# Kernel tuning notes

Hardware: AMD Instinct MI355X
Metric: run time of the kernel (lower is better)

Reference implementation:

```python
import jax, jax.numpy as jnp
import numpy as np

B, T, C, H = 2, 2048, 1024, 16

def setup_inputs() -> dict:
    key = jax.random.key(0)
    ks = jax.random.split(key, 6)
    s = 1.0 / np.sqrt(C)
    return {
        "x": jax.random.normal(ks[0], (B, T, C), jnp.float32),
        "Wq": jax.random.normal(ks[1], (C, C), jnp.float32) * s,
        "Wk": jax.random.normal(ks[2], (C, C), jnp.float32) * s,
        "Wv": jax.random.normal(ks[3], (C, C), jnp.float32) * s,
        "Wp": jax.random.normal(ks[4], (C, C), jnp.float32) * s,
        "bp": jnp.zeros((C,), jnp.float32),
    }

def reference(x, Wq, Wk, Wv, Wp, bp):
    b, t, c = x.shape
    hd = c // H  # head dim
    # Linear layers: torch nn.Linear computes x @ W.T
    def split_heads(y):
        return y.reshape(b, t, H, hd).transpose(0, 2, 1, 3)  # [B,H,T,hd]
    q = split_heads(x @ Wq.T)
    k = split_heads(x @ Wk.T)
    v = split_heads(x @ Wv.T)
    scale = hd ** -0.5
    wei = jnp.einsum('bhqd,bhkd->bhqk', q, k) * scale  # [B,H,T,T]
    causal = jnp.tril(jnp.ones((t, t), bool))
    wei = jnp.where(causal, wei, -jnp.inf)
    wei = jax.nn.softmax(wei, axis=-1)
    out = jnp.einsum('bhqk,bhkd->bhqd', wei, v)  # [B,H,T,hd]
    out = out.transpose(0, 2, 1, 3).reshape(b, t, c)
    return out @ Wp.T + bp
```

## Files before the change

### kernel.cpp

```cpp
#include <hip/hip_runtime.h>
#include <hip/hip_bf16.h>
#include <stdint.h>

#define B_ 2
#define T_ 2048
#define C_ 1024
#define H_ 16
#define HD_ 64
#define NTOK (B_*T_)

typedef __bf16 bf16;
typedef bf16 bf16x4 __attribute__((ext_vector_type(4)));
typedef bf16 bf16x8 __attribute__((ext_vector_type(8)));
typedef float f32x4 __attribute__((ext_vector_type(4)));

static __device__ __forceinline__ f32x4 mfma16(bf16x8 a, bf16x8 b, f32x4 c) {
  return __builtin_amdgcn_mfma_f32_16x16x32_bf16(a, b, c, 0, 0, 0);
}

static __device__ __forceinline__ void gload_lds16(const void* g, void* l) {
  __builtin_amdgcn_global_load_lds(
      (__attribute__((address_space(1))) void*)g,
      (__attribute__((address_space(3))) void*)l, 16, 0, 0);
}

static __device__ __forceinline__ uint32_t cvt_pk_bf16(float lo, float hi) {
  uint32_t r;
  asm("v_cvt_pk_bf16_f32 %0, %1, %2" : "=v"(r) : "v"(lo), "v"(hi));
  return r;
}

__global__ void cvt_f32_bf16(const float* __restrict__ src, bf16* __restrict__ dst, int n4) {
  int i = blockIdx.x * blockDim.x + threadIdx.x;
  if (i >= n4) return;
  float4 v = reinterpret_cast<const float4*>(src)[i];
  bf16x4 o;
  o.x = (bf16)v.x; o.y = (bf16)v.y; o.z = (bf16)v.z; o.w = (bf16)v.w;
  reinterpret_cast<bf16x4*>(dst)[i] = o;
}

__global__ void cvt4_f32_bf16(const float* __restrict__ s0, const float* __restrict__ s1,
                              const float* __restrict__ s2, const float* __restrict__ s3,
                              bf16* __restrict__ d0, bf16* __restrict__ d1,
                              bf16* __restrict__ d2, bf16* __restrict__ d3, int n4) {
  int i = blockIdx.x * blockDim.x + threadIdx.x;
  if (i >= n4) return;
  const float* src = (blockIdx.y == 0) ? s0 : (blockIdx.y == 1) ? s1 : (blockIdx.y == 2) ? s2 : s3;
  bf16* dst = (blockIdx.y == 0) ? d0 : (blockIdx.y == 1) ? d1 : (blockIdx.y == 2) ? d2 : d3;
  float4 v = reinterpret_cast<const float4*>(src)[i];
  bf16x4 o;
  o.x = (bf16)v.x; o.y = (bf16)v.y; o.z = (bf16)v.z; o.w = (bf16)v.w;
  reinterpret_cast<bf16x4*>(dst)[i] = o;
}

__global__ __launch_bounds__(256) void qkv_gemm(
    const bf16* __restrict__ X,
    const bf16* __restrict__ Wq, const bf16* __restrict__ Wk, const bf16* __restrict__ Wv,
    bf16* __restrict__ Q, bf16* __restrict__ K, bf16* __restrict__ VT) {
  __shared__ bf16 As[128 * 32];
  __shared__ bf16 Bs[128 * 32];
  const int z = blockIdx.z;
  const bf16* W = (z == 0) ? Wq : (z == 1) ? Wk : Wv;
  const int n0 = blockIdx.x * 128;
  const int o0 = blockIdx.y * 128;
  const int tid = threadIdx.x;
  const int lane = tid & 63;
  const int w = tid >> 6;
  const int wr = w >> 1, wc = w & 1;
  const int l15 = lane & 15, lhi = lane >> 4;

  f32x4 acc[4][4] = {};

  const int ca = tid;
  const int cb = tid + 256;
  const int rowa = ca >> 2, cola = (ca & 3) * 8;
  const int rowb = cb >> 2, colb = (cb & 3) * 8;

  for (int k0 = 0; k0 < C_; k0 += 32) {
    __syncthreads();
    gload_lds16(X + (size_t)(n0 + rowa) * C_ + k0 + cola, (char*)As + ca * 16);
    gload_lds16(X + (size_t)(n0 + rowb) * C_ + k0 + colb, (char*)As + cb * 16);
    gload_lds16(W + (size_t)(o0 + rowa) * C_ + k0 + cola, (char*)Bs + ca * 16);
    gload_lds16(W + (size_t)(o0 + rowb) * C_ + k0 + colb, (char*)Bs + cb * 16);
    __syncthreads();
    bf16x8 a[4], b[4];
#pragma unroll
    for (int m = 0; m < 4; m++)
      a[m] = *reinterpret_cast<const bf16x8*>(&As[(wr * 64 + m * 16 + l15) * 32 + lhi * 8]);
#pragma unroll
    for (int n = 0; n < 4; n++)
      b[n] = *reinterpret_cast<const bf16x8*>(&Bs[(wc * 64 + n * 16 + l15) * 32 + lhi * 8]);
#pragma unroll
    for (int m = 0; m < 4; m++)
#pragma unroll
      for (int n = 0; n < 4; n++)
        acc[m][n] = mfma16(a[m], b[n], acc[m][n]);
  }

  const float QSCALE = 0.125f * 1.44269504f;
#pragma unroll
  for (int m = 0; m < 4; m++) {
#pragma unroll
    for (int n = 0; n < 4; n++) {
#pragma unroll
      for (int r = 0; r < 4; r++) {
        int tok = n0 + wr * 64 + m * 16 + lhi * 4 + r;
        int o = o0 + wc * 64 + n * 16 + l15;
        int bb = tok >> 11, t = tok & (T_ - 1);
        int h = o >> 6, d = o & 63;
        float v = acc[m][n][r];
        if (z == 0) {
          Q[((size_t)(bb * H_ + h) * T_ + t) * HD_ + d] = (bf16)(v * QSCALE);
        } else if (z == 1) {
          K[((size_t)(bb * H_ + h) * T_ + t) * HD_ + d] = (bf16)v;
        } else {
          VT[((size_t)(bb * H_ + h) * HD_ + d) * T_ + t] = (bf16)v;
        }
      }
    }
  }
}

__global__ __launch_bounds__(256, 3) void attn_kernel(
    const bf16* __restrict__ Q, const bf16* __restrict__ K,
    const bf16* __restrict__ VT, bf16* __restrict__ att) {
  __shared__ bf16 Kt[2][64 * 64];
  __shared__ bf16 Vt[2][64 * 64];
  __shared__ bf16 P[4][32][72];
  const int tid = threadIdx.x;
  const int lane = tid & 63;
  const int w = tid >> 6;
  const int l15 = lane & 15, lhi = lane >> 4;
  const int bh = blockIdx.x;
  const int b = bh >> 4, h = bh & 15;
  const int qt = (int)gridDim.y - 1 - (int)blockIdx.y;
  const int qw0 = qt * 128 + w * 32;
  const bf16* Qb = Q + (size_t)bh * T_ * HD_;
  const bf16* Kb = K + (size_t)bh * T_ * HD_;
  const bf16* Vb = VT + (size_t)bh * HD_ * T_;

  bf16x8 q[2][2];
#pragma unroll
  for (int m = 0; m < 2; m++)
#pragma unroll
    for (int kk = 0; kk < 2; kk++)
      q[m][kk] = *reinterpret_cast<const bf16x8*>(
          &Qb[(size_t)(qw0 + m * 16 + l15) * HD_ + kk * 32 + lhi * 8]);

  f32x4 o_acc[2][4] = {};
  float lsum[2] = {0.f, 0.f};

  const int nt = 2 * qt + 2;

  const int c0 = tid, c1 = tid + 256;
  const int r0 = c0 >> 3, x0 = (c0 & 7) ^ (r0 & 7);
  const int r1 = c1 >> 3, x1 = (c1 & 7) ^ (r1 & 7);

#define STAGE(tt, bb)                                                                \
  do {                                                                               \
    int kv = (tt) * 64;                                                              \
    gload_lds16(Kb + (size_t)(kv + r0) * HD_ + x0 * 8, (char*)&Kt[bb][0] + c0 * 16); \
    gload_lds16(Kb + (size_t)(kv + r1) * HD_ + x1 * 8, (char*)&Kt[bb][0] + c1 * 16); \
    gload_lds16(Vb + (size_t)r0 * T_ + kv + x0 * 8, (char*)&Vt[bb][0] + c0 * 16);    \
    gload_lds16(Vb + (size_t)r1 * T_ + kv + x1 * 8, (char*)&Vt[bb][0] + c1 * 16);    \
  } while (0)

  STAGE(0, 0);
  __syncthreads();
  int cur = 0;

  for (int it = 0; it < nt; ++it) {
    const int kv0 = it * 64;
    if (it + 1 < nt) STAGE(it + 1, cur ^ 1);

    if (kv0 <= qw0 + 31) {
      f32x4 s[2][4] = {};
#pragma unroll
      for (int n = 0; n < 4; n++) {
        const int krow = n * 16 + l15;
#pragma unroll
        for (int kk = 0; kk < 2; kk++) {
          const int kx = (kk * 4 + lhi) ^ (l15 & 7);
          bf16x8 kf = *reinterpret_cast<const bf16x8*>(
              (const char*)&Kt[cur][0] + krow * 128 + kx * 16);
          s[0][n] = mfma16(kf, q[0][kk], s[0][n]);
          s[1][n] = mfma16(kf, q[1][kk], s[1][n]);
        }
      }

      if (kv0 + 63 > qw0) {
#pragma unroll
        for (int m = 0; m < 2; m++) {
          const int qrow = qw0 + m * 16 + l15;
#pragma unroll
          for (int n = 0; n < 4; n++) {
            const int key = kv0 + n * 16 + lhi * 4;
#pragma unroll
            for (int r = 0; r < 4; r++) {
              if (key + r > qrow) s[m][n][r] = -1e30f;
            }
          }
        }
      }
#pragma unroll
      for (int m = 0; m < 2; m++) {
        char* pw = (char*)&P[w][m * 16 + l15][0];
#pragma unroll
        for (int n = 0; n < 4; n++) {
          float p0 = __builtin_amdgcn_exp2f(s[m][n][0]);
          float p1 = __builtin_amdgcn_exp2f(s[m][n][1]);
          float p2 = __builtin_amdgcn_exp2f(s[m][n][2]);
          float p3 = __builtin_amdgcn_exp2f(s[m][n][3]);
          lsum[m] += (p0 + p1) + (p2 + p3);
          uint32_t lo = cvt_pk_bf16(p0, p1);
          uint32_t hi = cvt_pk_bf16(p2, p3);
          *reinterpret_cast<uint2*>(pw + (4 * n + lhi) * 8) = make_uint2(lo, hi);
        }
      }
      bf16x8 pa[2][2];
#pragma unroll
      for (int m = 0; m < 2; m++)
#pragma unroll
        for (int kk = 0; kk < 2; kk++)
          pa[m][kk] = *reinterpret_cast<const bf16x8*>(
              (const char*)&P[w][m * 16 + l15][0] + kk * 64 + lhi * 16);
#pragma unroll
      for (int n = 0; n < 4; n++) {
        const int vrow = n * 16 + l15;
#pragma unroll
        for (int kk = 0; kk < 2; kk++) {
          const int vx = (kk * 4 + lhi) ^ (l15 & 7);
          bf16x8 vf = *reinterpret_cast<const bf16x8*>(
              (const char*)&Vt[cur][0] + vrow * 128 + vx * 16);
          o_acc[0][n] = mfma16(pa[0][kk], vf, o_acc[0][n]);
          o_acc[1][n] = mfma16(pa[1][kk], vf, o_acc[1][n]);
        }
      }
    }
    __syncthreads();
    cur ^= 1;
  }
#undef STAGE

  float lred[2];
#pragma unroll
  for (int m = 0; m < 2; m++) {
    float v = lsum[m];
    v += __shfl_xor(v, 16);
    v += __shfl_xor(v, 32);
    lred[m] = v;
  }
#pragma unroll
  for (int m = 0; m < 2; m++) {
#pragma unroll
    for (int r = 0; r < 4; r++) {
      float rs = __shfl(lred[m], (lane & 48) + lhi * 4 + r);
      float li = 1.f / rs;
      int t = qw0 + m * 16 + lhi * 4 + r;
#pragma unroll
      for (int n = 0; n < 4; n++) {
        int d = n * 16 + l15;
        att[((size_t)(b * T_ + t) * H_ + h) * HD_ + d] = (bf16)(o_acc[m][n][r] * li);
      }
    }
  }
}

__global__ __launch_bounds__(256) void proj_gemm(
    const bf16* __restrict__ A, const bf16* __restrict__ Wp,
    const float* __restrict__ bp, float* __restrict__ out) {
  __shared__ bf16 As[128 * 32];
  __shared__ bf16 Bs[128 * 32];
  const int n0 = blockIdx.x * 128;
  const int o0 = blockIdx.y * 128;
  const int tid = threadIdx.x;
  const int lane = tid & 63;
  const int w = tid >> 6;
  const int wr = w >> 1, wc = w & 1;
  const int l15 = lane & 15, lhi = lane >> 4;

  f32x4 acc[4][4] = {};

  const int ca = tid;
  const int cb = tid + 256;
  const int rowa = ca >> 2, cola = (ca & 3) * 8;
  const int rowb = cb >> 2, colb = (cb & 3) * 8;

  for (int k0 = 0; k0 < C_; k0 += 32) {
    __syncthreads();
    gload_lds16(A + (size_t)(n0 + rowa) * C_ + k0 + cola, (char*)As + ca * 16);
    gload_lds16(A + (size_t)(n0 + rowb) * C_ + k0 + colb, (char*)As + cb * 16);
    gload_lds16(Wp + (size_t)(o0 + rowa) * C_ + k0 + cola, (char*)Bs + ca * 16);
    gload_lds16(Wp + (size_t)(o0 + rowb) * C_ + k0 + colb, (char*)Bs + cb * 16);
    __syncthreads();
    bf16x8 a[4], b[4];
#pragma unroll
    for (int m = 0; m < 4; m++)
      a[m] = *reinterpret_cast<const bf16x8*>(&As[(wr * 64 + m * 16 + l15) * 32 + lhi * 8]);
#pragma unroll
    for (int n = 0; n < 4; n++)
      b[n] = *reinterpret_cast<const bf16x8*>(&Bs[(wc * 64 + n * 16 + l15) * 32 + lhi * 8]);
#pragma unroll
    for (int m = 0; m < 4; m++)
#pragma unroll
      for (int n = 0; n < 4; n++)
        acc[m][n] = mfma16(a[m], b[n], acc[m][n]);
  }

#pragma unroll
  for (int m = 0; m < 4; m++) {
#pragma unroll
    for (int n = 0; n < 4; n++) {
#pragma unroll
      for (int r = 0; r < 4; r++) {
        int tok = n0 + wr * 64 + m * 16 + lhi * 4 + r;
        int o = o0 + wc * 64 + n * 16 + l15;
        out[(size_t)tok * C_ + o] = acc[m][n][r] + bp[o];
      }
    }
  }
}

extern "C" void kernel_launch(void* const* d_in, const int* in_sizes, int n_in,
                              void* d_out, int out_size, void* d_ws, size_t ws_size,
                              hipStream_t stream) {
  const float* x  = (const float*)d_in[0];
  const float* Wq = (const float*)d_in[1];
  const float* Wk = (const float*)d_in[2];
  const float* Wv = (const float*)d_in[3];
  const float* Wp = (const float*)d_in[4];
  const float* bp = (const float*)d_in[5];
  float* out = (float*)d_out;

  char* ws = (char*)d_ws;
  size_t off = 0;
  bf16* xb  = (bf16*)(ws + off); off += (size_t)NTOK * C_ * 2;
  bf16* wqb = (bf16*)(ws + off); off += (size_t)C_ * C_ * 2;
  bf16* wkb = (bf16*)(ws + off); off += (size_t)C_ * C_ * 2;
  bf16* wvb = (bf16*)(ws + off); off += (size_t)C_ * C_ * 2;
  bf16* wpb = (bf16*)(ws + off); off += (size_t)C_ * C_ * 2;
  bf16* Qd  = (bf16*)(ws + off); off += (size_t)NTOK * C_ * 2;
  bf16* Kd  = (bf16*)(ws + off); off += (size_t)NTOK * C_ * 2;
  bf16* VTd = (bf16*)(ws + off); off += (size_t)NTOK * C_ * 2;
  bf16* att = (bf16*)(ws + off); off += (size_t)NTOK * C_ * 2;
  (void)ws_size; (void)out_size; (void)in_sizes; (void)n_in;

  int n4 = NTOK * C_ / 4;
  cvt_f32_bf16<<<(n4 + 255) / 256, 256, 0, stream>>>(x, xb, n4);
  n4 = C_ * C_ / 4;
  cvt4_f32_bf16<<<dim3((n4 + 255) / 256, 4), 256, 0, stream>>>(
      Wq, Wk, Wv, Wp, wqb, wkb, wvb, wpb, n4);

  qkv_gemm<<<dim3(NTOK / 128, C_ / 128, 3), 256, 0, stream>>>(xb, wqb, wkb, wvb, Qd, Kd, VTd);
  attn_kernel<<<dim3(B_ * H_, T_ / 128), 256, 0, stream>>>(Qd, Kd, VTd, att);
  proj_gemm<<<dim3(NTOK / 128, C_ / 128), 256, 0, stream>>>(att, wpb, bp, out);
}
```

Measured before the change: 115.9 us.

## Split causal attention KV range across blocks with atomic accumulation, merge conversion kernels

Causal attention is split along the KV dimension into chunks of up to 8 tiles, so long query tiles are spread over several blocks. This balances the triangular workload and gives a grid of 40x32 blocks instead of 16x32. Partial outputs and row sums go to fp32 buffers through atomic adds, and a new normalization kernel writes the bf16 output. The two fp32-to-bf16 conversion kernels are merged into one launch. The split adds a memset, extra fp32 atomic traffic and one more kernel launch. It appears to rely on no max-subtraction in the softmax, since partial sums are added without rescaling.

Measured after the change: 130.6 us. +12.7%, slower.

```diff
diff --git a/kernel.cpp b/kernel.cpp
--- a/kernel.cpp
+++ b/kernel.cpp
@@ -30,27 +30,27 @@
   return r;
 }
 
-__global__ void cvt_f32_bf16(const float* __restrict__ src, bf16* __restrict__ dst, int n4) {
-  int i = blockIdx.x * blockDim.x + threadIdx.x;
-  if (i >= n4) return;
-  float4 v = reinterpret_cast<const float4*>(src)[i];
+__global__ void cvt_all(const float* __restrict__ x,
+                        const float* __restrict__ w0, const float* __restrict__ w1,
+                        const float* __restrict__ w2, const float* __restrict__ w3,
+                        bf16* __restrict__ xb,
+                        bf16* __restrict__ d0, bf16* __restrict__ d1,
+                        bf16* __restrict__ d2, bf16* __restrict__ d3) {
+  const int i = blockIdx.x * 256 + threadIdx.x;
+  const int y = blockIdx.y;
+  const float* src;
+  bf16* dst;
+  size_t off4 = 0;
+  if (y < 4) {
+    src = x; dst = xb; off4 = (size_t)y << 18;
+  } else if (y == 4) { src = w0; dst = d0; }
+  else if (y == 5)   { src = w1; dst = d1; }
+  else if (y == 6)   { src = w2; dst = d2; }
+  else               { src = w3; dst = d3; }
+  float4 v = reinterpret_cast<const float4*>(src)[off4 + i];
   bf16x4 o;
   o.x = (bf16)v.x; o.y = (bf16)v.y; o.z = (bf16)v.z; o.w = (bf16)v.w;
-  reinterpret_cast<bf16x4*>(dst)[i] = o;
-}
-
-__global__ void cvt4_f32_bf16(const float* __restrict__ s0, const float* __restrict__ s1,
-                              const float* __restrict__ s2, const float* __restrict__ s3,
-                              bf16* __restrict__ d0, bf16* __restrict__ d1,
-                              bf16* __restrict__ d2, bf16* __restrict__ d3, int n4) {
-  int i = blockIdx.x * blockDim.x + threadIdx.x;
-  if (i >= n4) return;
-  const float* src = (blockIdx.y == 0) ? s0 : (blockIdx.y == 1) ? s1 : (blockIdx.y == 2) ? s2 : s3;
-  bf16* dst = (blockIdx.y == 0) ? d0 : (blockIdx.y == 1) ? d1 : (blockIdx.y == 2) ? d2 : d3;
-  float4 v = reinterpret_cast<const float4*>(src)[i];
-  bf16x4 o;
-  o.x = (bf16)v.x; o.y = (bf16)v.y; o.z = (bf16)v.z; o.w = (bf16)v.w;
-  reinterpret_cast<bf16x4*>(dst)[i] = o;
+  reinterpret_cast<bf16x4*>(dst)[off4 + i] = o;
 }
 
 __global__ __launch_bounds__(256) void qkv_gemm(
@@ -121,9 +121,9 @@
   }
 }
 
-__global__ __launch_bounds__(256, 3) void attn_kernel(
+__global__ __launch_bounds__(256, 3) void attn_split(
     const bf16* __restrict__ Q, const bf16* __restrict__ K,
-    const bf16* __restrict__ VT, bf16* __restrict__ att) {
+    const bf16* __restrict__ VT, float* __restrict__ Oacc, float* __restrict__ Lacc) {
   __shared__ bf16 Kt[2][64 * 64];
   __shared__ bf16 Vt[2][64 * 64];
   __shared__ bf16 P[4][32][72];
@@ -131,14 +131,24 @@
   const int lane = tid & 63;
   const int w = tid >> 6;
   const int l15 = lane & 15, lhi = lane >> 4;
-  const int bh = blockIdx.x;
-  const int b = bh >> 4, h = bh & 15;
-  const int qt = (int)gridDim.y - 1 - (int)blockIdx.y;
+
+  const int x = blockIdx.x;
+  int qt, c0;
+  if (x < 4)       { qt = x;               c0 = 0; }
+  else if (x < 12) { qt = 4 + ((x - 4) >> 1);  c0 = (x - 4) & 1; }
+  else if (x < 24) { qt = 8 + (x - 12) / 3;    c0 = (x - 12) % 3; }
+  else             { qt = 12 + ((x - 24) >> 2); c0 = (x - 24) & 3; }
+
+  const int bh = blockIdx.y;
   const int qw0 = qt * 128 + w * 32;
   const bf16* Qb = Q + (size_t)bh * T_ * HD_;
   const bf16* Kb = K + (size_t)bh * T_ * HD_;
   const bf16* Vb = VT + (size_t)bh * HD_ * T_;
 
+  const int nt = 2 * qt + 2;
+  const int t0 = c0 * 8;
+  const int t1 = (t0 + 8 < nt) ? t0 + 8 : nt;
+
   bf16x8 q[2][2];
 #pragma unroll
   for (int m = 0; m < 2; m++)
@@ -150,28 +160,26 @@
   f32x4 o_acc[2][4] = {};
   float lsum[2] = {0.f, 0.f};
 
-  const int nt = 2 * qt + 2;
-
-  const int c0 = tid, c1 = tid + 256;
-  const int r0 = c0 >> 3, x0 = (c0 & 7) ^ (r0 & 7);
-  const int r1 = c1 >> 3, x1 = (c1 & 7) ^ (r1 & 7);
+  const int c0i = tid, c1i = tid + 256;
+  const int r0 = c0i >> 3, x0 = (c0i & 7) ^ (r0 & 7);
+  const int r1 = c1i >> 3, x1 = (c1i & 7) ^ (r1 & 7);
 
 #define STAGE(tt, bb)                                                                \
   do {                                                                               \
     int kv = (tt) * 64;                                                              \
-    gload_lds16(Kb + (size_t)(kv + r0) * HD_ + x0 * 8, (char*)&Kt[bb][0] + c0 * 16); \
-    gload_lds16(Kb + (size_t)(kv + r1) * HD_ + x1 * 8, (char*)&Kt[bb][0] + c1 * 16); \
-    gload_lds16(Vb + (size_t)r0 * T_ + kv + x0 * 8, (char*)&Vt[bb][0] + c0 * 16);    \
-    gload_lds16(Vb + (size_t)r1 * T_ + kv + x1 * 8, (char*)&Vt[bb][0] + c1 * 16);    \
+    gload_lds16(Kb + (size_t)(kv + r0) * HD_ + x0 * 8, (char*)&Kt[bb][0] + c0i * 16); \
+    gload_lds16(Kb + (size_t)(kv + r1) * HD_ + x1 * 8, (char*)&Kt[bb][0] + c1i * 16); \
+    gload_lds16(Vb + (size_t)r0 * T_ + kv + x0 * 8, (char*)&Vt[bb][0] + c0i * 16);   \
+    gload_lds16(Vb + (size_t)r1 * T_ + kv + x1 * 8, (char*)&Vt[bb][0] + c1i * 16);   \
   } while (0)
 
-  STAGE(0, 0);
+  STAGE(t0, 0);
   __syncthreads();
   int cur = 0;
 
-  for (int it = 0; it < nt; ++it) {
+  for (int it = t0; it < t1; ++it) {
     const int kv0 = it * 64;
-    if (it + 1 < nt) STAGE(it + 1, cur ^ 1);
+    if (it + 1 < t1) STAGE(it + 1, cur ^ 1);
 
     if (kv0 <= qw0 + 31) {
       f32x4 s[2][4] = {};
@@ -242,28 +250,42 @@
   }
 #undef STAGE
 
-  float lred[2];
-#pragma unroll
-  for (int m = 0; m < 2; m++) {
-    float v = lsum[m];
-    v += __shfl_xor(v, 16);
-    v += __shfl_xor(v, 32);
-    lred[m] = v;
-  }
-#pragma unroll
-  for (int m = 0; m < 2; m++) {
-#pragma unroll
-    for (int r = 0; r < 4; r++) {
-      float rs = __shfl(lred[m], (lane & 48) + lhi * 4 + r);
-      float li = 1.f / rs;
-      int t = qw0 + m * 16 + lhi * 4 + r;
+  if (t0 * 64 <= qw0 + 31) {
+#pragma unroll
+    for (int m = 0; m < 2; m++) {
+      float v = lsum[m];
+      v += __shfl_xor(v, 16);
+      v += __shfl_xor(v, 32);
+      if (lhi == 0) unsafeAtomicAdd(&Lacc[(size_t)bh * T_ + qw0 + m * 16 + l15], v);
+    }
+#pragma unroll
+    for (int m = 0; m < 2; m++) {
 #pragma unroll
       for (int n = 0; n < 4; n++) {
-        int d = n * 16 + l15;
-        att[((size_t)(b * T_ + t) * H_ + h) * HD_ + d] = (bf16)(o_acc[m][n][r] * li);
-      }
-    }
-  }
+#pragma unroll
+        for (int r = 0; r < 4; r++) {
+          int t = qw0 + m * 16 + lhi * 4 + r;
+          int d = n * 16 + l15;
+          unsafeAtomicAdd(&Oacc[((size_t)bh * T_ + t) * HD_ + d], o_acc[m][n][r]);
+        }
+      }
+    }
+  }
+}
+
+__global__ void attn_norm(const float* __restrict__ Oacc, const float* __restrict__ Lacc,
+                          bf16* __restrict__ att) {
+  const int tid = threadIdx.x;
+  const int row = blockIdx.x * 16 + (tid >> 4);
+  const int quad = tid & 15;
+  const float li = 1.f / Lacc[row];
+  float4 o = reinterpret_cast<const float4*>(Oacc)[(size_t)row * 16 + quad];
+  const int bh = row >> 11, t = row & (T_ - 1);
+  const int b = bh >> 4, h = bh & 15;
+  bf16x4 v;
+  v.x = (bf16)(o.x * li); v.y = (bf16)(o.y * li);
+  v.z = (bf16)(o.z * li); v.w = (bf16)(o.w * li);
+  *reinterpret_cast<bf16x4*>(&att[((size_t)(b * T_ + t) * H_ + h) * HD_ + quad * 4]) = v;
 }
 
 __global__ __launch_bounds__(256) void proj_gemm(
@@ -343,15 +365,16 @@
   bf16* Kd  = (bf16*)(ws + off); off += (size_t)NTOK * C_ * 2;
   bf16* VTd = (bf16*)(ws + off); off += (size_t)NTOK * C_ * 2;
   bf16* att = (bf16*)(ws + off); off += (size_t)NTOK * C_ * 2;
+  float* Oacc = (float*)(ws + off); off += (size_t)NTOK * C_ * 4;
+  float* Lacc = (float*)(ws + off); off += (size_t)B_ * H_ * T_ * 4;
   (void)ws_size; (void)out_size; (void)in_sizes; (void)n_in;
 
-  int n4 = NTOK * C_ / 4;
-  cvt_f32_bf16<<<(n4 + 255) / 256, 256, 0, stream>>>(x, xb, n4);
-  n4 = C_ * C_ / 4;
-  cvt4_f32_bf16<<<dim3((n4 + 255) / 256, 4), 256, 0, stream>>>(
-      Wq, Wk, Wv, Wp, wqb, wkb, wvb, wpb, n4);
+  hipMemsetAsync(Oacc, 0, (size_t)NTOK * C_ * 4 + (size_t)B_ * H_ * T_ * 4, stream);
+
+  cvt_all<<<dim3(1024, 8), 256, 0, stream>>>(x, Wq, Wk, Wv, Wp, xb, wqb, wkb, wvb, wpb);
 
   qkv_gemm<<<dim3(NTOK / 128, C_ / 128, 3), 256, 0, stream>>>(xb, wqb, wkb, wvb, Qd, Kd, VTd);
-  attn_kernel<<<dim3(B_ * H_, T_ / 128), 256, 0, stream>>>(Qd, Kd, VTd, att);
+  attn_split<<<dim3(40, B_ * H_), 256, 0, stream>>>(Qd, Kd, VTd, Oacc, Lacc);
+  attn_norm<<<dim3(B_ * H_ * T_ / 16), 256, 0, stream>>>(Oacc, Lacc, att);
   proj_gemm<<<dim3(NTOK / 128, C_ / 128), 256, 0, stream>>>(att, wpb, bp, out);
 }
```
